# Performance work log

Measured on AMD Instinct MI355X. Metric: run time of the kernel, lower is better.

## Reference

```python
import jax, jax.numpy as jnp
import numpy as np

VX, VY = 0.2, 0.2
X_MIN, Y_MIN = -51.2, -51.2
Z_MIN, Z_MAX = -3.0, 3.0
GX, GY = 512, 512
NVOX = GX * GY
Z_CENTER = 0.0  # z_min + vz/2 with vz = 6.0
EPS = 1e-3  # BN1d default eps in mmdet3d PFNLayer


def _voxel_ids(pts):
    # pts: [B, N, 3] -> integer pillar coords and flat ids
    ix = jnp.clip(jnp.floor((pts[..., 0] - X_MIN) / VX).astype(jnp.int32), 0, GX - 1)
    iy = jnp.clip(jnp.floor((pts[..., 1] - Y_MIN) / VY).astype(jnp.int32), 0, GY - 1)
    return ix, iy, ix * GY + iy


def _segment_mean(vals, ids, n):
    # vals: [N, C], ids: [N] -> [n, C] mean per segment (0 for empty)
    s = jax.ops.segment_sum(vals, ids, num_segments=n)
    c = jax.ops.segment_sum(jnp.ones(vals.shape[0], vals.dtype), ids, num_segments=n)
    return s / jnp.maximum(c, 1.0)[:, None]


def _pillar_grid(pts, W, gamma, beta, mean, var):
    # DynamicPillarFeatureNet: point aug -> linear -> BN(eval) -> relu -> scatter-mean
    ix, iy, vid = _voxel_ids(pts)  # [B, N]
    fdt = pts.dtype
    # cluster center: per-voxel mean of xyz, gathered back to points
    cluster_mean = jax.vmap(lambda p, i: _segment_mean(p, i, NVOX)[i])(pts, vid)  # [B,N,3]
    center = jnp.stack([
        (ix.astype(fdt) + 0.5) * VX + X_MIN,
        (iy.astype(fdt) + 0.5) * VY + Y_MIN,
        jnp.full(ix.shape, Z_CENTER, dtype=fdt),
    ], axis=-1)  # [B,N,3]
    f = jnp.concatenate([pts, pts - cluster_mean, pts - center], axis=-1)  # [B,N,9]
    h = jnp.einsum('bnf,fc->bnc', f, W)  # Linear(9 -> C), no bias (BN follows)
    h = jax.nn.relu(gamma * (h - mean) * jax.lax.rsqrt(var + EPS) + beta)  # [B,N,C]
    # scatter mean per pillar -> dense grid (zeros where empty)
    grid = jax.vmap(lambda v, i: _segment_mean(v, i, NVOX))(h, vid)  # [B, NVOX, C]
    return grid


def setup_inputs() -> dict:
    key = jax.random.key(0)
    k0, k1, kw = jax.random.split(key, 3)
    B, N, C = 2, 100000, 64
    lo = jnp.array([X_MIN, Y_MIN, Z_MIN], jnp.float32)
    hi = jnp.array([-X_MIN, -Y_MIN, Z_MAX], jnp.float32)
    pc0s = jax.random.uniform(k0, (B, N, 3), jnp.float32) * (hi - lo) + lo
    pc1s = jax.random.uniform(k1, (B, N, 3), jnp.float32) * (hi - lo) + lo
    W = jax.random.normal(kw, (9, C), jnp.float32) * (1.0 / np.sqrt(9.0))
    return {
        'pc0s': pc0s, 'pc1s': pc1s, 'W': W,
        'bn_gamma': jnp.ones((C,), jnp.float32),
        'bn_beta': jnp.zeros((C,), jnp.float32),
        'bn_mean': jnp.zeros((C,), jnp.float32),
        'bn_var': jnp.ones((C,), jnp.float32),
    }


def reference(pc0s, pc1s, W, bn_gamma, bn_beta, bn_mean, bn_var):
    g0 = _pillar_grid(pc0s, W, bn_gamma, bn_beta, bn_mean, bn_var)
    g1 = _pillar_grid(pc1s, W, bn_gamma, bn_beta, bn_mean, bn_var)
    # sparse_pc1 - sparse_pc0, coalesced: identical to dense grid difference
    diff = (g1 - g0).reshape(pc0s.shape[0], GX, GY, -1)  # [B, GX, GY, C]
    return diff
```

## Files before the change

### kernel.cpp

```cpp
#include <hip/hip_runtime.h>

#define VXC 0.2f
#define VYC 0.2f
#define XMINC -51.2f
#define YMINC -51.2f
#define GXD 512
#define GYD 512
#define NVOXD (GXD * GYD)
#define BN_EPS 1e-3f

__global__ void init_and_precompute(int* __restrict__ cnt, int nzero4,
                                    const float* __restrict__ W,
                                    const float* __restrict__ gamma,
                                    const float* __restrict__ beta,
                                    const float* __restrict__ mean,
                                    const float* __restrict__ var,
                                    float* __restrict__ P) {
    int nzero_blocks = (nzero4 + 255) / 256;
    if ((int)blockIdx.x < nzero_blocks) {
        int i = blockIdx.x * 256 + threadIdx.x;
        if (i < nzero4) ((int4*)cnt)[i] = make_int4(0, 0, 0, 0);
        return;
    }
    int c = threadIdx.x;
    if (c >= 64) return;
    float scale = gamma[c] * (1.0f / sqrtf(var[c] + BN_EPS));
    float w0 = W[0*64+c], w1 = W[1*64+c], w2 = W[2*64+c];
    float w3 = W[3*64+c], w4 = W[4*64+c], w5 = W[5*64+c];
    float w6 = W[6*64+c], w7 = W[7*64+c], w8 = W[8*64+c];
    P[0*64+c] = (w0 + w3 + w6) * scale;
    P[1*64+c] = (w1 + w4 + w7) * scale;
    P[2*64+c] = (w2 + w5 + w8) * scale;
    P[3*64+c] = w3 * scale;
    P[4*64+c] = w4 * scale;
    P[5*64+c] = w5 * scale;
    P[6*64+c] = w6 * scale;
    P[7*64+c] = w7 * scale;
    P[8*64+c] = beta[c] - mean[c] * scale;
}

__global__ void bin_points(const float* __restrict__ pc0, const float* __restrict__ pc1,
                           int* __restrict__ cnt, unsigned* __restrict__ pk_arr,
                           int B, int N) {
    int i = blockIdx.x * blockDim.x + threadIdx.x;
    int per_cloud = B * N;
    if (i >= 2 * per_cloud) return;
    int cloud = (i >= per_cloud) ? 1 : 0;
    int i2 = i - cloud * per_cloud;
    int b = i2 / N;
    const float* p = (cloud ? pc1 : pc0) + (size_t)i2 * 3;
    float x = p[0], y = p[1];
    int ix = (int)floorf((x - XMINC) / VXC); ix = min(max(ix, 0), GXD - 1);
    int iy = (int)floorf((y - YMINC) / VYC); iy = min(max(iy, 0), GYD - 1);
    int hidx = (cloud * B + b) * NVOXD + ix * GYD + iy;
    int pos = atomicAdd(cnt + hidx, 1);
    pk_arr[i] = ((unsigned)hidx << 8) | (unsigned)pos;
}

__global__ void scan_block(const int* __restrict__ in, int* __restrict__ out,
                           int* __restrict__ bsums) {
    int tid = threadIdx.x;
    size_t base = (size_t)blockIdx.x * 1024;
    int4 v = ((const int4*)(in + base))[tid];
    int t0 = v.x, t1 = t0 + v.y, t2 = t1 + v.z, t3 = t2 + v.w;
    __shared__ int lds[256];
    lds[tid] = t3;
    __syncthreads();
    for (int d = 1; d < 256; d <<= 1) {
        int t = (tid >= d) ? lds[tid - d] : 0;
        __syncthreads();
        lds[tid] += t;
        __syncthreads();
    }
    int excl = lds[tid] - t3;
    if (tid == 255) bsums[blockIdx.x] = lds[255];
    ((int4*)(out + base))[tid] = make_int4(excl, excl + t0, excl + t1, excl + t2);
}

__global__ void add_bases(int* __restrict__ off, const int* __restrict__ bases,
                          int n4, int total) {
    int i = blockIdx.x * blockDim.x + threadIdx.x;
    if (i >= n4) return;
    int4 v = ((int4*)off)[i];
    int b = bases[i >> 8];
    v.x += b; v.y += b; v.z += b; v.w += b;
    ((int4*)off)[i] = v;
    if (i == 0) off[n4 * 4] = total;
}

__global__ void scatter_csr(const float* __restrict__ pc0, const float* __restrict__ pc1,
                            const int* __restrict__ off, const unsigned* __restrict__ pk_arr,
                            float4* __restrict__ csr, int B, int N) {
    int i = blockIdx.x * blockDim.x + threadIdx.x;
    int per_cloud = B * N;
    if (i >= 2 * per_cloud) return;
    int cloud = (i >= per_cloud) ? 1 : 0;
    int i2 = i - cloud * per_cloud;
    const float* p = (cloud ? pc1 : pc0) + (size_t)i2 * 3;
    unsigned pk = pk_arr[i];
    int o = off[pk >> 8] + (int)(pk & 255u);
    csr[o] = make_float4(p[0], p[1], p[2], 0.0f);
}

__global__ void voxel_stats(const float4* __restrict__ csr, const int* __restrict__ off,
                            float4* __restrict__ stats, int n) {
    int i = blockIdx.x * blockDim.x + threadIdx.x;
    if (i >= n) return;
    int s = off[i], e = off[i + 1];
    float4 r = make_float4(0.0f, 0.0f, 0.0f, 0.0f);
    if (e > s) {
        float sx = 0.0f, sy = 0.0f, sz = 0.0f;
        for (int j = s; j < e; ++j) {
            float4 pt = csr[j];
            sx += pt.x; sy += pt.y; sz += pt.z;
        }
        float inv = 1.0f / (float)(e - s);
        r = make_float4(sx * inv, sy * inv, sz * inv, inv);
    }
    stats[i] = r;
}

__global__ __launch_bounds__(256)
void gather(const float4* __restrict__ csr, const int* __restrict__ off,
            const float4* __restrict__ stats, const float* __restrict__ P,
            float* __restrict__ out, int B) {
    int g = blockIdx.x * blockDim.x + threadIdx.x;
    int c = g & 63;
    int w = g >> 6;
    int nquad = (B * NVOXD) >> 2;
    if (w >= nquad) return;

    float A   = P[0*64+c], Bw  = P[1*64+c], Cw  = P[2*64+c];
    float w3s = P[3*64+c], w4s = P[4*64+c], w5s = P[5*64+c];
    float w6s = P[6*64+c], w7s = P[7*64+c], offc = P[8*64+c];
    int base1 = B * NVOXD;
    int bv0 = w << 2;

    int4 a0 = *(const int4*)(off + bv0);
    int4 a1 = *(const int4*)(off + base1 + bv0);
    int o0[5] = {a0.x, a0.y, a0.z, a0.w, off[bv0 + 4]};
    int o1[5] = {a1.x, a1.y, a1.z, a1.w, off[base1 + bv0 + 4]};

    #pragma unroll
    for (int q = 0; q < 4; ++q) {
        int bv = bv0 + q;
        int s0 = o0[q], e0 = o0[q + 1];
        int s1 = o1[q], e1 = o1[q + 1];
        float res = 0.0f;
        if (e0 > s0 || e1 > s1) {
            int v = bv & (NVOXD - 1);
            int ix = v >> 9, iy = v & 511;
            float cx = ((float)ix + 0.5f) * VXC + XMINC;
            float cy = ((float)iy + 0.5f) * VYC + YMINC;
            float basef = offc - cx * w6s - cy * w7s;
            if (e0 > s0) {
                float4 st = stats[bv];
                float cbias = basef - st.x * w3s - st.y * w4s - st.z * w5s;
                float hsum = 0.0f;
                for (int j = s0; j < e0; ++j) {
                    float4 pt = csr[j];
                    hsum += fmaxf(pt.x * A + pt.y * Bw + pt.z * Cw + cbias, 0.0f);
                }
                res -= hsum * st.w;
            }
            if (e1 > s1) {
                float4 st = stats[base1 + bv];
                float cbias = basef - st.x * w3s - st.y * w4s - st.z * w5s;
                float hsum = 0.0f;
                for (int j = s1; j < e1; ++j) {
                    float4 pt = csr[j];
                    hsum += fmaxf(pt.x * A + pt.y * Bw + pt.z * Cw + cbias, 0.0f);
                }
                res += hsum * st.w;
            }
        }
        __builtin_nontemporal_store(res, out + ((size_t)bv << 6) + c);
    }
}

extern "C" void kernel_launch(void* const* d_in, const int* in_sizes, int n_in,
                              void* d_out, int out_size, void* d_ws, size_t ws_size,
                              hipStream_t stream) {
    const float* pc0   = (const float*)d_in[0];
    const float* pc1   = (const float*)d_in[1];
    const float* Wm    = (const float*)d_in[2];
    const float* gamma = (const float*)d_in[3];
    const float* beta  = (const float*)d_in[4];
    const float* mean  = (const float*)d_in[5];
    const float* var   = (const float*)d_in[6];
    float* out = (float*)d_out;

    int B = out_size / (NVOXD * 64);
    int N = in_sizes[0] / (3 * B);
    int npts = 2 * B * N;
    int n = 2 * B * NVOXD;
    int nblocks_scan = n / 1024;

    float4* csr   = (float4*)d_ws;
    float4* stats = csr + npts + 4;
    int* off      = (int*)(stats + n);
    int* aux      = off + n + 4;
    int* aux2     = aux + nblocks_scan;
    unsigned* pk  = (unsigned*)(aux2 + nblocks_scan);
    float* P      = (float*)(pk + npts);

    int nzero4 = n / 4;
    int nzero_blocks = (nzero4 + 255) / 256;
    init_and_precompute<<<nzero_blocks + 1, 256, 0, stream>>>(
        off, nzero4, Wm, gamma, beta, mean, var, P);

    int g1 = (npts + 255) / 256;
    bin_points<<<g1, 256, 0, stream>>>(pc0, pc1, off, pk, B, N);

    scan_block<<<nblocks_scan, 256, 0, stream>>>(off, off, aux);
    scan_block<<<1, 256, 0, stream>>>(aux, aux, aux2);
    add_bases<<<(n / 4 + 255) / 256, 256, 0, stream>>>(off, aux, n / 4, npts);

    scatter_csr<<<g1, 256, 0, stream>>>(pc0, pc1, off, pk, csr, B, N);

    voxel_stats<<<(n + 255) / 256, 256, 0, stream>>>(csr, off, stats, n);

    long long total_thr = ((long long)B * NVOXD >> 2) * 64;
    int g4 = (int)((total_thr + 255) / 256);
    gather<<<g4, 256, 0, stream>>>(csr, off, stats, P, out, B);
}
```

Measured before the change: 233.0 us.

## Fuse voxel stats into gather, vectorize binning, widen gather to 8 voxels

Removes the voxel_stats kernel and its stats buffer. Each gather lane now computes the per-voxel mean itself, with a fast path for single-point voxels that folds the cluster offset into the weights. bin_points and scatter_csr each handle four points per thread using float4 loads and uint4 packed keys. gather processes eight voxels per wavefront instead of four. The trade-off is that the per-voxel sums are recomputed in all 64 channel lanes, and the vectorized kernels assume N is divisible by 4.

```diff
diff --git a/kernel.cpp b/kernel.cpp
--- a/kernel.cpp
+++ b/kernel.cpp
@@ -40,21 +40,29 @@
 }
 
 __global__ void bin_points(const float* __restrict__ pc0, const float* __restrict__ pc1,
-                           int* __restrict__ cnt, unsigned* __restrict__ pk_arr,
+                           int* __restrict__ cnt, uint4* __restrict__ pk4,
                            int B, int N) {
     int i = blockIdx.x * blockDim.x + threadIdx.x;
-    int per_cloud = B * N;
-    if (i >= 2 * per_cloud) return;
-    int cloud = (i >= per_cloud) ? 1 : 0;
-    int i2 = i - cloud * per_cloud;
-    int b = i2 / N;
-    const float* p = (cloud ? pc1 : pc0) + (size_t)i2 * 3;
-    float x = p[0], y = p[1];
-    int ix = (int)floorf((x - XMINC) / VXC); ix = min(max(ix, 0), GXD - 1);
-    int iy = (int)floorf((y - YMINC) / VYC); iy = min(max(iy, 0), GYD - 1);
-    int hidx = (cloud * B + b) * NVOXD + ix * GYD + iy;
-    int pos = atomicAdd(cnt + hidx, 1);
-    pk_arr[i] = ((unsigned)hidx << 8) | (unsigned)pos;
+    int per4 = (B * N) >> 2;
+    if (i >= 2 * per4) return;
+    int cloud = (i >= per4) ? 1 : 0;
+    int i2 = i - cloud * per4;
+    int b = i2 / (N >> 2);
+    const float4* p4 = (const float4*)(cloud ? pc1 : pc0) + (size_t)i2 * 3;
+    float4 q0 = p4[0], q1 = p4[1], q2 = p4[2];
+    float xs[4] = {q0.x, q0.w, q1.z, q2.y};
+    float ys[4] = {q0.y, q1.x, q1.w, q2.z};
+    int vbase = (cloud * B + b) * NVOXD;
+    unsigned r[4];
+    #pragma unroll
+    for (int k = 0; k < 4; ++k) {
+        int ix = (int)floorf((xs[k] - XMINC) / VXC); ix = min(max(ix, 0), GXD - 1);
+        int iy = (int)floorf((ys[k] - YMINC) / VYC); iy = min(max(iy, 0), GYD - 1);
+        int hidx = vbase + ix * GYD + iy;
+        int pos = atomicAdd(cnt + hidx, 1);
+        r[k] = ((unsigned)hidx << 8) | (unsigned)pos;
+    }
+    pk4[i] = make_uint4(r[0], r[1], r[2], r[3]);
 }
 
 __global__ void scan_block(const int* __restrict__ in, int* __restrict__ out,
@@ -89,60 +97,54 @@
 }
 
 __global__ void scatter_csr(const float* __restrict__ pc0, const float* __restrict__ pc1,
-                            const int* __restrict__ off, const unsigned* __restrict__ pk_arr,
+                            const int* __restrict__ off, const uint4* __restrict__ pk4,
                             float4* __restrict__ csr, int B, int N) {
     int i = blockIdx.x * blockDim.x + threadIdx.x;
-    int per_cloud = B * N;
-    if (i >= 2 * per_cloud) return;
-    int cloud = (i >= per_cloud) ? 1 : 0;
-    int i2 = i - cloud * per_cloud;
-    const float* p = (cloud ? pc1 : pc0) + (size_t)i2 * 3;
-    unsigned pk = pk_arr[i];
-    int o = off[pk >> 8] + (int)(pk & 255u);
-    csr[o] = make_float4(p[0], p[1], p[2], 0.0f);
-}
-
-__global__ void voxel_stats(const float4* __restrict__ csr, const int* __restrict__ off,
-                            float4* __restrict__ stats, int n) {
-    int i = blockIdx.x * blockDim.x + threadIdx.x;
-    if (i >= n) return;
-    int s = off[i], e = off[i + 1];
-    float4 r = make_float4(0.0f, 0.0f, 0.0f, 0.0f);
-    if (e > s) {
-        float sx = 0.0f, sy = 0.0f, sz = 0.0f;
-        for (int j = s; j < e; ++j) {
-            float4 pt = csr[j];
-            sx += pt.x; sy += pt.y; sz += pt.z;
-        }
-        float inv = 1.0f / (float)(e - s);
-        r = make_float4(sx * inv, sy * inv, sz * inv, inv);
-    }
-    stats[i] = r;
+    int per4 = (B * N) >> 2;
+    if (i >= 2 * per4) return;
+    int cloud = (i >= per4) ? 1 : 0;
+    int i2 = i - cloud * per4;
+    const float4* p4 = (const float4*)(cloud ? pc1 : pc0) + (size_t)i2 * 3;
+    float4 q0 = p4[0], q1 = p4[1], q2 = p4[2];
+    uint4 pkv = pk4[i];
+    float xs[4] = {q0.x, q0.w, q1.z, q2.y};
+    float ys[4] = {q0.y, q1.x, q1.w, q2.z};
+    float zs[4] = {q0.z, q1.y, q2.x, q2.w};
+    unsigned pr[4] = {pkv.x, pkv.y, pkv.z, pkv.w};
+    #pragma unroll
+    for (int k = 0; k < 4; ++k) {
+        int o = off[pr[k] >> 8] + (int)(pr[k] & 255u);
+        csr[o] = make_float4(xs[k], ys[k], zs[k], 0.0f);
+    }
 }
 
 __global__ __launch_bounds__(256)
 void gather(const float4* __restrict__ csr, const int* __restrict__ off,
-            const float4* __restrict__ stats, const float* __restrict__ P,
-            float* __restrict__ out, int B) {
+            const float* __restrict__ P, float* __restrict__ out, int B) {
     int g = blockIdx.x * blockDim.x + threadIdx.x;
     int c = g & 63;
     int w = g >> 6;
-    int nquad = (B * NVOXD) >> 2;
-    if (w >= nquad) return;
+    int noct = (B * NVOXD) >> 3;
+    if (w >= noct) return;
 
     float A   = P[0*64+c], Bw  = P[1*64+c], Cw  = P[2*64+c];
     float w3s = P[3*64+c], w4s = P[4*64+c], w5s = P[5*64+c];
     float w6s = P[6*64+c], w7s = P[7*64+c], offc = P[8*64+c];
+    float A1 = A - w3s, B1 = Bw - w4s, C1 = Cw - w5s;
     int base1 = B * NVOXD;
-    int bv0 = w << 2;
-
-    int4 a0 = *(const int4*)(off + bv0);
-    int4 a1 = *(const int4*)(off + base1 + bv0);
-    int o0[5] = {a0.x, a0.y, a0.z, a0.w, off[bv0 + 4]};
-    int o1[5] = {a1.x, a1.y, a1.z, a1.w, off[base1 + bv0 + 4]};
+    int bv0 = w << 3;
+
+    int4 a0  = *(const int4*)(off + bv0);
+    int4 a0b = *(const int4*)(off + bv0 + 4);
+    int4 a1  = *(const int4*)(off + base1 + bv0);
+    int4 a1b = *(const int4*)(off + base1 + bv0 + 4);
+    int o0[9] = {a0.x, a0.y, a0.z, a0.w, a0b.x, a0b.y, a0b.z, a0b.w,
+                 off[bv0 + 8]};
+    int o1[9] = {a1.x, a1.y, a1.z, a1.w, a1b.x, a1b.y, a1b.z, a1b.w,
+                 off[base1 + bv0 + 8]};
 
     #pragma unroll
-    for (int q = 0; q < 4; ++q) {
+    for (int q = 0; q < 8; ++q) {
         int bv = bv0 + q;
         int s0 = o0[q], e0 = o0[q + 1];
         int s1 = o1[q], e1 = o1[q + 1];
@@ -153,25 +155,43 @@
             float cx = ((float)ix + 0.5f) * VXC + XMINC;
             float cy = ((float)iy + 0.5f) * VYC + YMINC;
             float basef = offc - cx * w6s - cy * w7s;
-            if (e0 > s0) {
-                float4 st = stats[bv];
-                float cbias = basef - st.x * w3s - st.y * w4s - st.z * w5s;
+            int n0 = e0 - s0;
+            if (n0 == 1) {
+                float4 pt = csr[s0];
+                res -= fmaxf(pt.x * A1 + pt.y * B1 + pt.z * C1 + basef, 0.0f);
+            } else if (n0 > 1) {
+                float sx = 0.0f, sy = 0.0f, sz = 0.0f;
+                for (int j = s0; j < e0; ++j) {
+                    float4 pt = csr[j];
+                    sx += pt.x; sy += pt.y; sz += pt.z;
+                }
+                float inv = 1.0f / (float)n0;
+                float cbias = basef - (sx * w3s + sy * w4s + sz * w5s) * inv;
                 float hsum = 0.0f;
                 for (int j = s0; j < e0; ++j) {
                     float4 pt = csr[j];
                     hsum += fmaxf(pt.x * A + pt.y * Bw + pt.z * Cw + cbias, 0.0f);
                 }
-                res -= hsum * st.w;
+                res -= hsum * inv;
             }
-            if (e1 > s1) {
-                float4 st = stats[base1 + bv];
-                float cbias = basef - st.x * w3s - st.y * w4s - st.z * w5s;
+            int n1 = e1 - s1;
+            if (n1 == 1) {
+                float4 pt = csr[s1];
+                res += fmaxf(pt.x * A1 + pt.y * B1 + pt.z * C1 + basef, 0.0f);
+            } else if (n1 > 1) {
+                float sx = 0.0f, sy = 0.0f, sz = 0.0f;
+                for (int j = s1; j < e1; ++j) {
+                    float4 pt = csr[j];
+                    sx += pt.x; sy += pt.y; sz += pt.z;
+                }
+                float inv = 1.0f / (float)n1;
+                float cbias = basef - (sx * w3s + sy * w4s + sz * w5s) * inv;
                 float hsum = 0.0f;
                 for (int j = s1; j < e1; ++j) {
                     float4 pt = csr[j];
                     hsum += fmaxf(pt.x * A + pt.y * Bw + pt.z * Cw + cbias, 0.0f);
                 }
-                res += hsum * st.w;
+                res += hsum * inv;
             }
         }
         __builtin_nontemporal_store(res, out + ((size_t)bv << 6) + c);
@@ -197,8 +217,7 @@
     int nblocks_scan = n / 1024;
 
     float4* csr   = (float4*)d_ws;
-    float4* stats = csr + npts + 4;
-    int* off      = (int*)(stats + n);
+    int* off      = (int*)(csr + npts + 4);
     int* aux      = off + n + 4;
     int* aux2     = aux + nblocks_scan;
     unsigned* pk  = (unsigned*)(aux2 + nblocks_scan);
@@ -209,18 +228,17 @@
     init_and_precompute<<<nzero_blocks + 1, 256, 0, stream>>>(
         off, nzero4, Wm, gamma, beta, mean, var, P);
 
-    int g1 = (npts + 255) / 256;
-    bin_points<<<g1, 256, 0, stream>>>(pc0, pc1, off, pk, B, N);
+    int nq = npts / 4;
+    int g1 = (nq + 255) / 256;
+    bin_points<<<g1, 256, 0, stream>>>(pc0, pc1, off, (uint4*)pk, B, N);
 
     scan_block<<<nblocks_scan, 256, 0, stream>>>(off, off, aux);
     scan_block<<<1, 256, 0, stream>>>(aux, aux, aux2);
     add_bases<<<(n / 4 + 255) / 256, 256, 0, stream>>>(off, aux, n / 4, npts);
 
-    scatter_csr<<<g1, 256, 0, stream>>>(pc0, pc1, off, pk, csr, B, N);
-
-    voxel_stats<<<(n + 255) / 256, 256, 0, stream>>>(csr, off, stats, n);
-
-    long long total_thr = ((long long)B * NVOXD >> 2) * 64;
+    scatter_csr<<<g1, 256, 0, stream>>>(pc0, pc1, off, (const uint4*)pk, csr, B, N);
+
+    long long total_thr = ((long long)B * NVOXD >> 3) * 64;
     int g4 = (int)((total_thr + 255) / 256);
-    gather<<<g4, 256, 0, stream>>>(csr, off, stats, P, out, B);
-}
+    gather<<<g4, 256, 0, stream>>>(csr, off, P, out, B);
+}
```

Result: faster. 215.0 us (-7.7%).
